# Kernel optimization log

Measured on AMD Instinct MI355X. Metric: run time of the kernel, lower is better.

The kernel has to match this reference:

```python
import jax, jax.numpy as jnp
import numpy as np

DIM, WIDTH, POOL, BATCH, SEQ = 4096, 4, 512, 256, 16

def setup_inputs() -> dict:
    key = jax.random.key(0)
    k1, k2, k3, k4 = jax.random.split(key, 4)
    x = jax.random.normal(k1, (BATCH, SEQ, DIM), dtype=jnp.float32)
    conv_state = jax.random.normal(k2, (POOL, WIDTH - 1, DIM), dtype=jnp.float32)
    weight = jax.random.normal(k3, (WIDTH, DIM), dtype=jnp.float32)
    bias = jax.random.normal(k4, (DIM,), dtype=jnp.float32)
    conv_state_indices = jnp.arange(BATCH, dtype=jnp.int32)
    return {"x": x, "conv_state": conv_state, "weight": weight,
            "bias": bias, "conv_state_indices": conv_state_indices}

def reference(x, conv_state, weight, bias, conv_state_indices):
    # x: [b, s, d]; conv_state: [pool, width-1, d]; weight: [width, d]
    b, s, d = x.shape
    width = weight.shape[0]
    state = conv_state[conv_state_indices]            # gather: [b, width-1, d]
    x_new = jnp.concatenate([state, x], axis=1)       # [b, width-1+s, d]
    # depthwise causal conv, width taps (small fixed loop over taps)
    out = bias
    for k in range(width):
        out = out + x_new[:, k:k + s, :] * weight[k]  # [b, s, d]
    out = jax.nn.silu(out)                            # activation=True
    new_state = x_new[:, -(width - 1):, :]            # [b, width-1, d]
    updated_conv_state = conv_state.at[conv_state_indices].set(new_state)
    return out, updated_conv_state
```

## Files before the change

kernel.cpp:

```cpp
#include <hip/hip_runtime.h>

constexpr int DIM   = 4096;
constexpr int WIDTH = 4;
constexpr int POOL  = 512;
constexpr int BATCH = 256;
constexpr int SEQ   = 16;

__global__ __launch_bounds__(256) void copy_state_kernel(
    const float4* __restrict__ src, float4* __restrict__ dst, int n4)
{
    int i = blockIdx.x * blockDim.x + threadIdx.x;
    const int stride = gridDim.x * blockDim.x;
    for (; i < n4; i += stride) dst[i] = src[i];
}

__global__ __launch_bounds__(256) void conv_silu_kernel(
    const float* __restrict__ x,
    const float* __restrict__ conv_state,
    const float* __restrict__ weight,
    const float* __restrict__ bias,
    const int*   __restrict__ idxs,
    float*       __restrict__ out,
    float*       __restrict__ out_state)
{
    const int b = blockIdx.y;
    const int d = (blockIdx.x * 256 + threadIdx.x) * 4;
    const int idx = idxs[b];

    float4 w[WIDTH];
#pragma unroll
    for (int k = 0; k < WIDTH; ++k)
        w[k] = *reinterpret_cast<const float4*>(weight + (size_t)k * DIM + d);
    const float4 bs = *reinterpret_cast<const float4*>(bias + d);

    float4 win[WIDTH];
#pragma unroll
    for (int t = 0; t < WIDTH - 1; ++t)
        win[t] = *reinterpret_cast<const float4*>(
            conv_state + ((size_t)idx * (WIDTH - 1) + t) * DIM + d);

    const float* xb = x   + (size_t)b * SEQ * DIM + d;
    float*       ob = out + (size_t)b * SEQ * DIM + d;

    for (int s = 0; s < SEQ; ++s) {
        win[WIDTH - 1] = *reinterpret_cast<const float4*>(xb + (size_t)s * DIM);

        float4 acc = bs;
#pragma unroll
        for (int k = 0; k < WIDTH; ++k) {
            acc.x += win[k].x * w[k].x;
            acc.y += win[k].y * w[k].y;
            acc.z += win[k].z * w[k].z;
            acc.w += win[k].w * w[k].w;
        }
        acc.x = acc.x / (1.0f + expf(-acc.x));
        acc.y = acc.y / (1.0f + expf(-acc.y));
        acc.z = acc.z / (1.0f + expf(-acc.z));
        acc.w = acc.w / (1.0f + expf(-acc.w));

        *reinterpret_cast<float4*>(ob + (size_t)s * DIM) = acc;

#pragma unroll
        for (int t = 0; t < WIDTH - 1; ++t) win[t] = win[t + 1];
    }

#pragma unroll
    for (int t = 0; t < WIDTH - 1; ++t)
        *reinterpret_cast<float4*>(
            out_state + ((size_t)idx * (WIDTH - 1) + t) * DIM + d) = win[t];
}

extern "C" void kernel_launch(void* const* d_in, const int* in_sizes, int n_in,
                              void* d_out, int out_size, void* d_ws, size_t ws_size,
                              hipStream_t stream)
{
    const float* x          = (const float*)d_in[0];
    const float* conv_state = (const float*)d_in[1];
    const float* weight     = (const float*)d_in[2];
    const float* bias       = (const float*)d_in[3];
    const int*   idxs       = (const int*)  d_in[4];

    float* out       = (float*)d_out;
    float* out_state = out + (size_t)BATCH * SEQ * DIM;

    const int n4 = POOL * (WIDTH - 1) * DIM / 4;
    copy_state_kernel<<<2048, 256, 0, stream>>>(
        (const float4*)conv_state, (float4*)out_state, n4);

    dim3 grid(DIM / (4 * 256), BATCH);
    conv_silu_kernel<<<grid, 256, 0, stream>>>(
        x, conv_state, weight, bias, idxs, out, out_state);
}
```

Measured before the change: 38.31 us.

## Fuse state copy into conv kernel and skip rows overwritten by batch

Merges the full conv_state copy kernel and the conv+SiLU kernel into one launch. Extra blocks copy the pool rows, and each one skips its row when some batch index targets it, because that row is rewritten by the conv path anyway. This removes a kernel launch, the ordering dependency between the two kernels, and roughly half of the redundant state copy traffic. The skip check reads idxs[threadIdx.x], which assumes BATCH equals the block size of 256; it also fully unrolls the seq loop.

```diff
diff --git a/kernel.cpp b/kernel.cpp
--- a/kernel.cpp
+++ b/kernel.cpp
@@ -6,15 +6,11 @@
 constexpr int BATCH = 256;
 constexpr int SEQ   = 16;
 
-__global__ __launch_bounds__(256) void copy_state_kernel(
-    const float4* __restrict__ src, float4* __restrict__ dst, int n4)
-{
-    int i = blockIdx.x * blockDim.x + threadIdx.x;
-    const int stride = gridDim.x * blockDim.x;
-    for (; i < n4; i += stride) dst[i] = src[i];
-}
+constexpr int D4_CHUNKS    = DIM / (4 * 256);
+constexpr int CONV_BLOCKS  = D4_CHUNKS * BATCH;
+constexpr int TOTAL_BLOCKS = CONV_BLOCKS + POOL;
 
-__global__ __launch_bounds__(256) void conv_silu_kernel(
+__global__ __launch_bounds__(256) void fused_conv_update_kernel(
     const float* __restrict__ x,
     const float* __restrict__ conv_state,
     const float* __restrict__ weight,
@@ -23,51 +19,76 @@
     float*       __restrict__ out,
     float*       __restrict__ out_state)
 {
-    const int b = blockIdx.y;
-    const int d = (blockIdx.x * 256 + threadIdx.x) * 4;
-    const int idx = idxs[b];
+    const int blk = blockIdx.x;
 
-    float4 w[WIDTH];
+    if (blk < CONV_BLOCKS) {
+        const int b     = blk >> 2;
+        const int chunk = blk & (D4_CHUNKS - 1);
+        const int d     = (chunk * 256 + threadIdx.x) * 4;
+        const int idx   = idxs[b];
+
+        float4 w[WIDTH];
 #pragma unroll
-    for (int k = 0; k < WIDTH; ++k)
-        w[k] = *reinterpret_cast<const float4*>(weight + (size_t)k * DIM + d);
-    const float4 bs = *reinterpret_cast<const float4*>(bias + d);
+        for (int k = 0; k < WIDTH; ++k)
+            w[k] = *reinterpret_cast<const float4*>(weight + (size_t)k * DIM + d);
+        const float4 bs = *reinterpret_cast<const float4*>(bias + d);
 
-    float4 win[WIDTH];
+        float4 win[WIDTH];
 #pragma unroll
-    for (int t = 0; t < WIDTH - 1; ++t)
-        win[t] = *reinterpret_cast<const float4*>(
-            conv_state + ((size_t)idx * (WIDTH - 1) + t) * DIM + d);
+        for (int t = 0; t < WIDTH - 1; ++t)
+            win[t] = *reinterpret_cast<const float4*>(
+                conv_state + ((size_t)idx * (WIDTH - 1) + t) * DIM + d);
 
-    const float* xb = x   + (size_t)b * SEQ * DIM + d;
-    float*       ob = out + (size_t)b * SEQ * DIM + d;
-
-    for (int s = 0; s < SEQ; ++s) {
-        win[WIDTH - 1] = *reinterpret_cast<const float4*>(xb + (size_t)s * DIM);
-
-        float4 acc = bs;
-#pragma unroll
-        for (int k = 0; k < WIDTH; ++k) {
-            acc.x += win[k].x * w[k].x;
-            acc.y += win[k].y * w[k].y;
-            acc.z += win[k].z * w[k].z;
-            acc.w += win[k].w * w[k].w;
-        }
-        acc.x = acc.x / (1.0f + expf(-acc.x));
-        acc.y = acc.y / (1.0f + expf(-acc.y));
-        acc.z = acc.z / (1.0f + expf(-acc.z));
-        acc.w = acc.w / (1.0f + expf(-acc.w));
-
-        *reinterpret_cast<float4*>(ob + (size_t)s * DIM) = acc;
+        const float* xb = x   + (size_t)b * SEQ * DIM + d;
+        float*       ob = out + (size_t)b * SEQ * DIM + d;
 
 #pragma unroll
-        for (int t = 0; t < WIDTH - 1; ++t) win[t] = win[t + 1];
-    }
+        for (int s = 0; s < SEQ; ++s) {
+            win[WIDTH - 1] = *reinterpret_cast<const float4*>(xb + (size_t)s * DIM);
+
+            float4 acc = bs;
+#pragma unroll
+            for (int k = 0; k < WIDTH; ++k) {
+                acc.x += win[k].x * w[k].x;
+                acc.y += win[k].y * w[k].y;
+                acc.z += win[k].z * w[k].z;
+                acc.w += win[k].w * w[k].w;
+            }
+            acc.x = acc.x / (1.0f + expf(-acc.x));
+            acc.y = acc.y / (1.0f + expf(-acc.y));
+            acc.z = acc.z / (1.0f + expf(-acc.z));
+            acc.w = acc.w / (1.0f + expf(-acc.w));
+
+            *reinterpret_cast<float4*>(ob + (size_t)s * DIM) = acc;
 
 #pragma unroll
-    for (int t = 0; t < WIDTH - 1; ++t)
-        *reinterpret_cast<float4*>(
-            out_state + ((size_t)idx * (WIDTH - 1) + t) * DIM + d) = win[t];
+            for (int t = 0; t < WIDTH - 1; ++t) win[t] = win[t + 1];
+        }
+
+#pragma unroll
+        for (int t = 0; t < WIDTH - 1; ++t)
+            *reinterpret_cast<float4*>(
+                out_state + ((size_t)idx * (WIDTH - 1) + t) * DIM + d) = win[t];
+    } else {
+        const int row = blk - CONV_BLOCKS;
+
+        __shared__ int skip;
+        if (threadIdx.x == 0) skip = 0;
+        __syncthreads();
+        if (idxs[threadIdx.x] == row) skip = 1;
+        __syncthreads();
+        if (skip) return;
+
+        const float4* src = reinterpret_cast<const float4*>(
+            conv_state + (size_t)row * (WIDTH - 1) * DIM);
+        float4* dst = reinterpret_cast<float4*>(
+            out_state + (size_t)row * (WIDTH - 1) * DIM);
+
+        constexpr int ROW_F4 = (WIDTH - 1) * DIM / 4;
+#pragma unroll
+        for (int i = threadIdx.x; i < ROW_F4; i += 256)
+            dst[i] = src[i];
+    }
 }
 
 extern "C" void kernel_launch(void* const* d_in, const int* in_sizes, int n_in,
@@ -83,11 +104,6 @@
     float* out       = (float*)d_out;
     float* out_state = out + (size_t)BATCH * SEQ * DIM;
 
-    const int n4 = POOL * (WIDTH - 1) * DIM / 4;
-    copy_state_kernel<<<2048, 256, 0, stream>>>(
-        (const float4*)conv_state, (float4*)out_state, n4);
-
-    dim3 grid(DIM / (4 * 256), BATCH);
-    conv_silu_kernel<<<grid, 256, 0, stream>>>(
+    fused_conv_update_kernel<<<TOTAL_BLOCKS, 256, 0, stream>>>(
         x, conv_state, weight, bias, idxs, out, out_state);
 }
```

New measurement: 33.49 us. 1.14x faster.
